# Kernel optimization log

Measured on AMD Instinct MI355X. Metric: run time of the kernel, lower is better.

The kernel has to match this reference:

```python
import jax, jax.numpy as jnp
import numpy as np

N, E, T, CIN, COUT = 20000, 160000, 8, 64, 128


def setup_inputs() -> dict:
    key = jax.random.key(0)
    ks = jax.random.split(key, 8)
    x = jax.random.normal(ks[0], (T, N, CIN), jnp.float32)
    edge_index = jax.random.randint(ks[1], (2, E), 0, N)
    edge_weight = jax.random.normal(ks[2], (E,), jnp.float32)
    # temporal Conv1d: kernel 3, xavier-ish small init (gain=0.1 in source)
    tconv_w = jax.random.normal(ks[3], (COUT, CIN, 3), jnp.float32) * 0.02
    tconv_b = jnp.zeros((COUT,), jnp.float32)
    ln_g = jnp.ones((COUT,), jnp.float32)
    ln_b = jnp.zeros((COUT,), jnp.float32)
    # residual 1x1 Conv1d (in != out channels)
    res_w = jax.random.normal(ks[4], (COUT, CIN), jnp.float32) * 0.05
    res_b = jnp.zeros((COUT,), jnp.float32)
    # GCNConv linear weight [out, in] and bias
    gcn_w = jax.random.normal(ks[5], (COUT, COUT), jnp.float32) * 0.05
    gcn_b = jnp.zeros((COUT,), jnp.float32)
    return dict(x=x, edge_index=edge_index, edge_weight=edge_weight,
                tconv_w=tconv_w, tconv_b=tconv_b, ln_g=ln_g, ln_b=ln_b,
                res_w=res_w, res_b=res_b, gcn_w=gcn_w, gcn_b=gcn_b)


def reference(x, edge_index, edge_weight, tconv_w, tconv_b, ln_g, ln_b,
              res_w, res_b, gcn_w, gcn_b):
    Tn, Nn, _ = x.shape
    xc = jnp.transpose(x, (1, 2, 0))  # [N, Cin, T]
    # temporal conv over T (kernel 3, pad 1)
    h = jax.lax.conv_general_dilated(
        xc, tconv_w, window_strides=(1,), padding=[(1, 1)],
        dimension_numbers=('NCH', 'OIH', 'NCH')) + tconv_b[None, :, None]
    h = jnp.transpose(h, (0, 2, 1))  # [N, T, Cout]
    # LayerNorm over channel dim
    mu = h.mean(-1, keepdims=True)
    var = ((h - mu) ** 2).mean(-1, keepdims=True)
    h = (h - mu) * jax.lax.rsqrt(var + 1e-5) * ln_g + ln_b
    h = jax.nn.relu(h)
    # 1x1 residual conv: [N,Cin,T] x [Cout,Cin] -> [N,T,Cout]
    res = jnp.einsum('nct,oc->nto', xc, res_w) + res_b
    xcmb = h + res  # [N, T, Cout]
    # --- GCNConv (PyG): softmax edge weights, self-loops, sym-normalize ---
    ew = jax.nn.softmax(edge_weight)  # softmax over all edges (dim=0)
    row, col = edge_index[0], edge_index[1]
    sl = jnp.arange(Nn)
    row_f = jnp.concatenate([row, sl])
    col_f = jnp.concatenate([col, sl])
    w_f = jnp.concatenate([ew, jnp.ones((Nn,), ew.dtype)])  # self-loop weight 1
    deg = jax.ops.segment_sum(w_f, col_f, num_segments=Nn)
    dinv = jnp.where(deg > 0, jax.lax.rsqrt(jnp.maximum(deg, 1e-12)), 0.0)
    norm = dinv[row_f] * w_f * dinv[col_f]  # [E+N]
    xt = jnp.einsum('ntc,oc->nto', xcmb, gcn_w)  # linear transform, all T at once
    msg = norm[:, None, None] * xt[row_f]        # gather sources: [E+N, T, Cout]
    agg = jax.ops.segment_sum(msg, col_f, num_segments=Nn) + gcn_b
    out = jax.nn.relu(agg)  # [N, T, Cout]
    return jnp.transpose(out, (1, 0, 2))  # [T, N, Cout] == stacked per-t list
```

## Files before the change

### kernel.cpp

```cpp
#include <hip/hip_runtime.h>
#include <math.h>

#define N_NODES 20000
#define E_EDGES 160000
#define T_STEPS 8
#define C_IN    64
#define C_OUT   128

typedef __bf16 bf16x8 __attribute__((ext_vector_type(8)));
typedef float  f32x4  __attribute__((ext_vector_type(4)));
#define MFMA16(a, b, c) __builtin_amdgcn_mfma_f32_16x16x32_bf16((a), (b), (c), 0, 0, 0)

__device__ __forceinline__ unsigned short f2u(float f) {
  __bf16 b = (__bf16)f;
  return __builtin_bit_cast(unsigned short, b);
}
__device__ __forceinline__ unsigned int pack2(float lo, float hi) {
  return (unsigned int)f2u(lo) | ((unsigned int)f2u(hi) << 16);
}

__device__ __forceinline__ float wredSum(float v) {
#pragma unroll
  for (int d = 32; d > 0; d >>= 1) v += __shfl_xor(v, d, 64);
  return v;
}
__device__ __forceinline__ float wredMax(float v) {
#pragma unroll
  for (int d = 32; d > 0; d >>= 1) v = fmaxf(v, __shfl_xor(v, d, 64));
  return v;
}
__device__ __forceinline__ int wredSumI(int v) {
#pragma unroll
  for (int d = 32; d > 0; d >>= 1) v += __shfl_xor(v, d, 64);
  return v;
}
__device__ __forceinline__ float bredSum(float v, float* sm4) {
  __syncthreads();
  v = wredSum(v);
  const int lane = threadIdx.x & 63, wid = threadIdx.x >> 6;
  if (lane == 0) sm4[wid] = v;
  __syncthreads();
  return sm4[0] + sm4[1] + sm4[2] + sm4[3];
}
__device__ __forceinline__ float bredMax(float v, float* sm4) {
  __syncthreads();
  v = wredMax(v);
  const int lane = threadIdx.x & 63, wid = threadIdx.x >> 6;
  if (lane == 0) sm4[wid] = v;
  __syncthreads();
  return fmaxf(fmaxf(sm4[0], sm4[1]), fmaxf(sm4[2], sm4[3]));
}
__device__ __forceinline__ int bredSumI(int v, int* sm4) {
  __syncthreads();
  v = wredSumI(v);
  const int lane = threadIdx.x & 63, wid = threadIdx.x >> 6;
  if (lane == 0) sm4[wid] = v;
  __syncthreads();
  return sm4[0] + sm4[1] + sm4[2] + sm4[3];
}

__global__ __launch_bounds__(256) void k_esoft(const float* __restrict__ w,
                                               float* __restrict__ pm, float* __restrict__ ps) {
  __shared__ float sm4[4];
  float m = -3.4e38f, s = 0.f;
  for (int i = blockIdx.x * 256 + threadIdx.x; i < E_EDGES; i += 256 * 256) {
    const float xw = w[i];
    if (xw > m) { s = s * expf(m - xw) + 1.f; m = xw; }
    else        { s += expf(xw - m); }
  }
  const float M = bredMax(m, sm4);
  const float sp = (s > 0.f) ? s * expf(m - M) : 0.f;
  const float S = bredSum(sp, sm4);
  if (threadIdx.x == 0) { pm[blockIdx.x] = M; ps[blockIdx.x] = S; }
}

__global__ __launch_bounds__(256) void k_edge(const float* __restrict__ w, const int* __restrict__ ei,
                                              const float* __restrict__ pm, const float* __restrict__ ps,
                                              float* __restrict__ ewv, float* __restrict__ deg,
                                              int* __restrict__ cnt) {
  __shared__ float sm4[4];
  const float mloc = pm[threadIdx.x];
  const float mx   = bredMax(mloc, sm4);
  const float sp   = ps[threadIdx.x] * expf(mloc - mx);
  const float sum  = bredSum(sp, sm4);
  const int e = blockIdx.x * 256 + threadIdx.x;
  const float v = expf(w[e] - mx) / sum;
  ewv[e] = v;
  const int c = ei[E_EDGES + e];
  atomicAdd(&deg[c], v);
  atomicAdd(&cnt[c], 1);
}

__global__ __launch_bounds__(256) void k_scan2(const int* __restrict__ cnt, const float* __restrict__ deg,
                                               float* __restrict__ dinv, int* __restrict__ off,
                                               int* __restrict__ cursor) {
  __shared__ int smI[4];
  __shared__ int wpart[4];
  const int tid = threadIdx.x, lane = tid & 63, wid = tid >> 6;
  const int i = blockIdx.x * 256 + tid;
  if (i < N_NODES) dinv[i] = rsqrtf(deg[i]);
  int part = 0;
  const int lim = blockIdx.x * 256;
  for (int j = tid; j < lim; j += 256) part += cnt[j];
  const int base = bredSumI(part, smI);
  const int v = (i < N_NODES) ? cnt[i] : 0;
  int s = v;
#pragma unroll
  for (int d = 1; d < 64; d <<= 1) { const int u = __shfl_up(s, d, 64); if (lane >= d) s += u; }
  if (lane == 63) wpart[wid] = s;
  __syncthreads();
  int add = base;
#pragma unroll
  for (int wv = 0; wv < 4; ++wv) if (wv < wid) add += wpart[wv];
  if (i < N_NODES) { const int excl = add + (s - v); off[i] = excl; cursor[i] = excl; }
  if (i == N_NODES - 1) off[N_NODES] = E_EDGES;
}

__global__ __launch_bounds__(256) void k_norm_scatter(const int* __restrict__ ei, const float* __restrict__ ewv,
                                                      const float* __restrict__ dinv, const float* __restrict__ qsc,
                                                      int* __restrict__ cursor, uint2* __restrict__ srcnrm) {
  const int e = blockIdx.x * 256 + threadIdx.x;
  const int r = ei[e], c = ei[E_EDGES + e];
  const float mul = dinv[r] * ewv[e] * dinv[c] * qsc[r];
  const int pos = atomicAdd(&cursor[c], 1);
  srcnrm[pos] = make_uint2((unsigned int)r, __builtin_bit_cast(unsigned int, mul));
}

__global__ __launch_bounds__(256) void k_wprep(const float* __restrict__ tconv_w, const float* __restrict__ res_w,
                                               const float* __restrict__ gcn_w, unsigned int* __restrict__ Bf,
                                               float* __restrict__ deg, int* __restrict__ cnt) {
  const int gid = blockIdx.x * 256 + threadIdx.x;
  if (gid < N_NODES) { deg[gid] = 1.0f; cnt[gid] = 0; }
  float v0, v1;
  if (gid < 12288) {
    const int reg = gid & 3, l = (gid >> 2) & 63, ct = (gid >> 8) & 7, ks = gid >> 11;
    const int o = ct * 16 + (l & 15);
    const int k0 = ks * 32 + ((l >> 4) & 3) * 8 + reg * 2;
    const int c0 = k0 & 63, tap0 = k0 >> 6;
    const int c1 = (k0 + 1) & 63, tap1 = (k0 + 1) >> 6;
    v0 = tconv_w[o * 192 + c0 * 3 + tap0];
    v1 = tconv_w[o * 192 + c1 * 3 + tap1];
  } else if (gid < 16384) {
    const int g = gid - 12288;
    const int reg = g & 3, l = (g >> 2) & 63, ct = (g >> 8) & 7, ks = g >> 11;
    const int o = ct * 16 + (l & 15);
    const int k0 = ks * 32 + ((l >> 4) & 3) * 8 + reg * 2;
    v0 = res_w[o * 64 + k0];
    v1 = res_w[o * 64 + k0 + 1];
  } else {
    const int g = gid - 16384;
    const int reg = g & 3, l = (g >> 2) & 63, ct = (g >> 8) & 7, ks = g >> 11;
    const int o = ct * 16 + (l & 15);
    const int k0 = ks * 32 + ((l >> 4) & 3) * 8 + reg * 2;
    v0 = gcn_w[o * 128 + k0];
    v1 = gcn_w[o * 128 + k0 + 1];
  }
  Bf[gid] = pack2(v0, v1);
}

#define XS_NODE 720
#define XS_SLOT 72
#define AS2_STRIDE 136
__global__ __launch_bounds__(256, 2) void k_fuse(const float* __restrict__ x,
                                                 const float* __restrict__ tconv_b,
                                                 const float* __restrict__ ln_g, const float* __restrict__ ln_b,
                                                 const float* __restrict__ res_b,
                                                 const unsigned int* __restrict__ Bf,
                                                 unsigned char* __restrict__ xq,
                                                 float* __restrict__ qsc) {
  const int tid = threadIdx.x, lane = tid & 63, w = tid >> 6;
  const int l15 = lane & 15, lg = lane >> 4;
  const int n0 = blockIdx.x * 16;

  __shared__ __align__(16) unsigned short XsAs[128 * AS2_STRIDE];
  unsigned short* Xs  = XsAs;
  unsigned short* As2 = XsAs;
  __shared__ float psum[4][128], psq[4][128];
  __shared__ float smu[128], srs[128];
  __shared__ unsigned int nmax[16];

  if (tid < 16) nmax[tid] = 0u;

#pragma unroll
  for (int p = 0; p < 8; ++p) {
    const int chunk = p * 256 + tid;
    const int tq = chunk >> 8, nn = (chunk >> 4) & 15, c4 = chunk & 15;
    const float4 v = *(const float4*)(x + ((size_t)tq * N_NODES + n0 + nn) * C_IN + c4 * 4);
    uint2 pk; pk.x = pack2(v.x, v.y); pk.y = pack2(v.z, v.w);
    *(uint2*)&Xs[nn * XS_NODE + (tq + 1) * XS_SLOT + c4 * 4] = pk;
  }
#pragma unroll
  for (int p = 0; p < 3; ++p) {
    const int i = p * 256 + tid;
    if (i < 576) {
      const int nn = i / 36;
      const int r = i - nn * 36;
      const int sl = (r < 18) ? 0 : 9;
      const int of = ((r < 18) ? r : r - 18) * 4;
      *(uint2*)&Xs[nn * XS_NODE + sl * XS_SLOT + of] = make_uint2(0u, 0u);
    }
  }

  const uint4* Bf4 = (const uint4*)Bf;
  uint4 Bc[2][6], Br[2][2];
#pragma unroll
  for (int ct = 0; ct < 2; ++ct) {
    const int ctg = w * 2 + ct;
#pragma unroll
    for (int ks = 0; ks < 6; ++ks) Bc[ct][ks] = Bf4[(ks * 8 + ctg) * 64 + lane];
#pragma unroll
    for (int ks = 0; ks < 2; ++ks) Br[ct][ks] = Bf4[3072 + (ks * 8 + ctg) * 64 + lane];
  }
  float cb[2], rb[2], gv[2], bv[2];
#pragma unroll
  for (int ct = 0; ct < 2; ++ct) {
    const int col = w * 32 + ct * 16 + l15;
    cb[ct] = tconv_b[col]; rb[ct] = res_b[col]; gv[ct] = ln_g[col]; bv[ct] = ln_b[col];
  }
  __syncthreads();

  f32x4 accC[8][2], accR[8][2];
#pragma unroll
  for (int rt = 0; rt < 8; ++rt)
#pragma unroll
    for (int ct = 0; ct < 2; ++ct) { accC[rt][ct] = (f32x4)0.f; accR[rt][ct] = (f32x4)0.f; }

#pragma unroll
  for (int ks = 0; ks < 6; ++ks) {
    bf16x8 af[8];
    const int slot = (l15 & 7) + (ks >> 1);
    const int koff = slot * XS_SLOT + (ks & 1) * 32 + lg * 8;
#pragma unroll
    for (int rt = 0; rt < 8; ++rt) {
      const int node = rt * 2 + (l15 >> 3);
      af[rt] = *(const bf16x8*)&Xs[node * XS_NODE + koff];
    }
#pragma unroll
    for (int rt = 0; rt < 8; ++rt)
#pragma unroll
      for (int ct = 0; ct < 2; ++ct)
        accC[rt][ct] = MFMA16(af[rt], __builtin_bit_cast(bf16x8, Bc[ct][ks]), accC[rt][ct]);
    if (ks == 2 || ks == 3) {
#pragma unroll
      for (int rt = 0; rt < 8; ++rt)
#pragma unroll
        for (int ct = 0; ct < 2; ++ct)
          accR[rt][ct] = MFMA16(af[rt], __builtin_bit_cast(bf16x8, Br[ct][ks - 2]), accR[rt][ct]);
    }
  }

#pragma unroll
  for (int rt = 0; rt < 8; ++rt) {
    float s[4], s2[4];
#pragma unroll
    for (int j = 0; j < 4; ++j) {
      const float h0 = accC[rt][0][j] + cb[0];
      const float h1 = accC[rt][1][j] + cb[1];
      accC[rt][0][j] = h0; accC[rt][1][j] = h1;
      s[j] = h0 + h1; s2[j] = h0 * h0 + h1 * h1;
    }
#pragma unroll
    for (int d = 1; d < 16; d <<= 1)
#pragma unroll
      for (int j = 0; j < 4; ++j) { s[j] += __shfl_xor(s[j], d, 64); s2[j] += __shfl_xor(s2[j], d, 64); }
    if (l15 == 0)
#pragma unroll
      for (int j = 0; j < 4; ++j) {
        psum[w][rt * 16 + lg * 4 + j] = s[j];
        psq[w][rt * 16 + lg * 4 + j] = s2[j];
      }
  }
  __syncthreads();
  if (tid < 128) {
    const float S  = psum[0][tid] + psum[1][tid] + psum[2][tid] + psum[3][tid];
    const float S2 = psq[0][tid] + psq[1][tid] + psq[2][tid] + psq[3][tid];
    const float mu = S * (1.f / 128.f);
    const float var = S2 * (1.f / 128.f) - mu * mu;
    smu[tid] = mu; srs[tid] = rsqrtf(var + 1e-5f);
  }
  __syncthreads();

#pragma unroll
  for (int rt = 0; rt < 8; ++rt)
#pragma unroll
    for (int j = 0; j < 4; ++j) {
      const int row = rt * 16 + lg * 4 + j;
      const float mu = smu[row], rs = srs[row];
      const int sw = ((row >> 3) & 1) << 4;
#pragma unroll
      for (int ct = 0; ct < 2; ++ct) {
        float xc = (accC[rt][ct][j] - mu) * rs * gv[ct] + bv[ct];
        xc = fmaxf(xc, 0.f) + accR[rt][ct][j] + rb[ct];
        const int col = w * 32 + ct * 16 + l15;
        As2[row * AS2_STRIDE + (col ^ sw)] = f2u(xc);
      }
    }
  __syncthreads();

  uint4 Bg[2][4];
#pragma unroll
  for (int ct = 0; ct < 2; ++ct)
#pragma unroll
    for (int ks = 0; ks < 4; ++ks) Bg[ct][ks] = Bf4[4096 + (ks * 8 + (w * 2 + ct)) * 64 + lane];

  f32x4 acc[8][2];
#pragma unroll
  for (int rt = 0; rt < 8; ++rt)
#pragma unroll
    for (int ct = 0; ct < 2; ++ct) acc[rt][ct] = (f32x4)0.f;

  const int swr = ((l15 >> 3) & 1) << 4;
#pragma unroll
  for (int ks = 0; ks < 4; ++ks) {
    bf16x8 af[8];
    const int koff = (ks * 32 + lg * 8) ^ swr;
#pragma unroll
    for (int rt = 0; rt < 8; ++rt)
      af[rt] = *(const bf16x8*)&As2[(rt * 16 + l15) * AS2_STRIDE + koff];
#pragma unroll
    for (int rt = 0; rt < 8; ++rt)
#pragma unroll
      for (int ct = 0; ct < 2; ++ct)
        acc[rt][ct] = MFMA16(af[rt], __builtin_bit_cast(bf16x8, Bg[ct][ks]), acc[rt][ct]);
  }

#pragma unroll
  for (int rt = 0; rt < 8; ++rt) {
    const int nn = rt * 2 + (lg >> 1);
    float m = 0.f;
#pragma unroll
    for (int ct = 0; ct < 2; ++ct)
#pragma unroll
      for (int j = 0; j < 4; ++j) m = fmaxf(m, fabsf(acc[rt][ct][j]));
    atomicMax(&nmax[nn], __builtin_bit_cast(unsigned int, m));
  }
  __syncthreads();
  if (tid < 16) qsc[n0 + tid] = __builtin_bit_cast(float, nmax[tid]) * (1.f / 127.f);

  const int t0 = (lg & 1) * 4;
#pragma unroll
  for (int rt = 0; rt < 8; ++rt) {
    const int nn = rt * 2 + (lg >> 1);
    const size_t n = (size_t)(n0 + nn);
    const float mx = __builtin_bit_cast(float, nmax[nn]);
    const float inv = (mx > 0.f) ? 127.f / mx : 0.f;
#pragma unroll
    for (int ct = 0; ct < 2; ++ct) {
      const int col = w * 32 + ct * 16 + l15;
      unsigned int pk8 = 0;
#pragma unroll
      for (int j = 0; j < 4; ++j) {
        const int q = (int)rintf(acc[rt][ct][j] * inv) + 128;
        pk8 |= ((unsigned int)q) << (8 * j);
      }
      *(unsigned int*)(xq + (n * C_OUT + col) * T_STEPS + t0) = pk8;
    }
  }
}

__global__ __launch_bounds__(256) void k_agg(const unsigned char* __restrict__ xq,
                                             const float* __restrict__ qsc,
                                             const uint2* __restrict__ srcnrm,
                                             const int* __restrict__ off, const float* __restrict__ dinv,
                                             const float* __restrict__ gcn_b, float* __restrict__ out) {
  const int tid = threadIdx.x, lane = tid & 63, w = tid >> 6;
  const int j = blockIdx.x * 4 + w;
  const int s = off[j], e = off[j + 1];
  const float d2 = dinv[j] * dinv[j];

  float acc[2][8];
#pragma unroll
  for (int h = 0; h < 2; ++h)
#pragma unroll
    for (int t = 0; t < 8; ++t) acc[h][t] = 0.f;

  float summul;
  {
    const float mul = d2 * qsc[j];
    summul = mul;
    const uint2 qa = *(const uint2*)(xq + ((size_t)j * C_OUT + lane) * T_STEPS);
    const uint2 qb = *(const uint2*)(xq + ((size_t)j * C_OUT + 64 + lane) * T_STEPS);
#pragma unroll
    for (int tt = 0; tt < 4; ++tt) {
      acc[0][tt]     = fmaf((float)((qa.x >> (8 * tt)) & 0xffu), mul, acc[0][tt]);
      acc[0][4 + tt] = fmaf((float)((qa.y >> (8 * tt)) & 0xffu), mul, acc[0][4 + tt]);
      acc[1][tt]     = fmaf((float)((qb.x >> (8 * tt)) & 0xffu), mul, acc[1][tt]);
      acc[1][4 + tt] = fmaf((float)((qb.y >> (8 * tt)) & 0xffu), mul, acc[1][4 + tt]);
    }
  }

  for (int cs = s; cs < e; cs += 64) {
    const uint2 sn = srcnrm[cs + lane];
    const int   rv = (int)sn.x;
    const float mv = __builtin_bit_cast(float, sn.y);
    const int cnt = min(64, e - cs);
    for (int k = 0; k < cnt; ++k) {
      const int   r   = __shfl(rv, k, 64);
      const float mul = __shfl(mv, k, 64);
      summul += mul;
      const uint2 qa = *(const uint2*)(xq + ((size_t)r * C_OUT + lane) * T_STEPS);
      const uint2 qb = *(const uint2*)(xq + ((size_t)r * C_OUT + 64 + lane) * T_STEPS);
#pragma unroll
      for (int tt = 0; tt < 4; ++tt) {
        acc[0][tt]     = fmaf((float)((qa.x >> (8 * tt)) & 0xffu), mul, acc[0][tt]);
        acc[0][4 + tt] = fmaf((float)((qa.y >> (8 * tt)) & 0xffu), mul, acc[0][4 + tt]);
        acc[1][tt]     = fmaf((float)((qb.x >> (8 * tt)) & 0xffu), mul, acc[1][tt]);
        acc[1][4 + tt] = fmaf((float)((qb.y >> (8 * tt)) & 0xffu), mul, acc[1][4 + tt]);
      }
    }
  }

  const float corr = 128.f * summul;
  const float b0 = gcn_b[lane], b1 = gcn_b[64 + lane];
#pragma unroll
  for (int h = 0; h < 2; ++h) {
    const float bo = h ? b1 : b0;
#pragma unroll
    for (int t = 0; t < 8; ++t) {
      const float v = acc[h][t] - corr + bo;
      out[((size_t)t * N_NODES + j) * C_OUT + h * 64 + lane] = fmaxf(v, 0.f);
    }
  }
}

extern "C" void kernel_launch(void* const* d_in, const int* in_sizes, int n_in,
                              void* d_out, int out_size, void* d_ws, size_t ws_size,
                              hipStream_t stream) {
  (void)in_sizes; (void)n_in; (void)out_size; (void)ws_size;
  const float* x       = (const float*)d_in[0];
  const int*   ei      = (const int*)d_in[1];
  const float* ewt     = (const float*)d_in[2];
  const float* tconv_w = (const float*)d_in[3];
  const float* tconv_b = (const float*)d_in[4];
  const float* ln_g    = (const float*)d_in[5];
  const float* ln_b    = (const float*)d_in[6];
  const float* res_w   = (const float*)d_in[7];
  const float* res_b   = (const float*)d_in[8];
  const float* gcn_w   = (const float*)d_in[9];
  const float* gcn_b   = (const float*)d_in[10];
  float* out = (float*)d_out;

  unsigned char* xq = (unsigned char*)d_ws;
  float* qsc  = (float*)(xq + (size_t)N_NODES * C_OUT * T_STEPS);
  unsigned int* Bf = (unsigned int*)(qsc + N_NODES);
  float* ewv   = (float*)(Bf + 24576);
  float* deg   = ewv + E_EDGES;
  float* dinv  = deg + N_NODES;
  float* pm    = dinv + N_NODES;
  float* ps    = pm + 256;
  int*   cnt    = (int*)(ps + 256);
  int*   off    = cnt + N_NODES;
  int*   cursor = off + N_NODES + 1;
  uint2* srcnrm = (uint2*)(((size_t)(cursor + N_NODES) + 15) & ~(size_t)15);

  const int nblk = (N_NODES + 255) / 256;
  const int eblk = E_EDGES / 256;

  k_wprep<<<96, 256, 0, stream>>>(tconv_w, res_w, gcn_w, Bf, deg, cnt);
  k_esoft<<<256, 256, 0, stream>>>(ewt, pm, ps);
  k_edge<<<eblk, 256, 0, stream>>>(ewt, ei, pm, ps, ewv, deg, cnt);
  k_scan2<<<nblk, 256, 0, stream>>>(cnt, deg, dinv, off, cursor);
  k_fuse<<<1250, 256, 0, stream>>>(x, tconv_b, ln_g, ln_b, res_b, Bf, xq, qsc);
  k_norm_scatter<<<eblk, 256, 0, stream>>>(ei, ewv, dinv, qsc, cursor, srcnrm);
  k_agg<<<N_NODES / 4, 256, 0, stream>>>(xq, qsc, srcnrm, off, dinv, gcn_b, out);
}
```

Measured before the change: 142.5 us.

## Fold residual conv into GCN weight, halve fuse tile, simplify agg loop

Precomputes W_gcn·W_res and W_gcn·res_b in the weight-prep kernel, so the residual branch is added inside the GCN GEMM and the separate residual accumulators and epilogue add go away. k_fuse now handles 8 nodes per block instead of 16 with separate Xs/As2 shared buffers, and launches twice as many blocks. The aggregation loop drops the shuffle-broadcast batching and loads each edge record directly. This cuts register and MFMA pressure in k_fuse and raises occupancy, at the cost of a serial per-thread 128-long dot product in the prep kernel and a change in bf16 rounding order.

```diff
diff --git a/kernel.cpp b/kernel.cpp
--- a/kernel.cpp
+++ b/kernel.cpp
@@ -127,10 +127,16 @@
 }
 
 __global__ __launch_bounds__(256) void k_wprep(const float* __restrict__ tconv_w, const float* __restrict__ res_w,
-                                               const float* __restrict__ gcn_w, unsigned int* __restrict__ Bf,
+                                               const float* __restrict__ gcn_w, const float* __restrict__ res_b,
+                                               unsigned int* __restrict__ Bf, float* __restrict__ c2,
                                                float* __restrict__ deg, int* __restrict__ cnt) {
   const int gid = blockIdx.x * 256 + threadIdx.x;
   if (gid < N_NODES) { deg[gid] = 1.0f; cnt[gid] = 0; }
+  if (gid < 128) {
+    float s = 0.f;
+    for (int o = 0; o < 128; ++o) s += gcn_w[gid * 128 + o] * res_b[o];
+    c2[gid] = s;
+  }
   float v0, v1;
   if (gid < 12288) {
     const int reg = gid & 3, l = (gid >> 2) & 63, ct = (gid >> 8) & 7, ks = gid >> 11;
@@ -143,10 +149,15 @@
   } else if (gid < 16384) {
     const int g = gid - 12288;
     const int reg = g & 3, l = (g >> 2) & 63, ct = (g >> 8) & 7, ks = g >> 11;
-    const int o = ct * 16 + (l & 15);
+    const int q = ct * 16 + (l & 15);
     const int k0 = ks * 32 + ((l >> 4) & 3) * 8 + reg * 2;
-    v0 = res_w[o * 64 + k0];
-    v1 = res_w[o * 64 + k0 + 1];
+    float a0 = 0.f, a1 = 0.f;
+    for (int o = 0; o < 128; ++o) {
+      const float gq = gcn_w[q * 128 + o];
+      a0 = fmaf(gq, res_w[o * 64 + k0], a0);
+      a1 = fmaf(gq, res_w[o * 64 + k0 + 1], a1);
+    }
+    v0 = a0; v1 = a1;
   } else {
     const int g = gid - 16384;
     const int reg = g & 3, l = (g >> 2) & 63, ct = (g >> 8) & 7, ks = g >> 11;
@@ -164,35 +175,34 @@
 __global__ __launch_bounds__(256, 2) void k_fuse(const float* __restrict__ x,
                                                  const float* __restrict__ tconv_b,
                                                  const float* __restrict__ ln_g, const float* __restrict__ ln_b,
-                                                 const float* __restrict__ res_b,
                                                  const unsigned int* __restrict__ Bf,
+                                                 const float* __restrict__ c2,
                                                  unsigned char* __restrict__ xq,
                                                  float* __restrict__ qsc) {
   const int tid = threadIdx.x, lane = tid & 63, w = tid >> 6;
   const int l15 = lane & 15, lg = lane >> 4;
-  const int n0 = blockIdx.x * 16;
-
-  __shared__ __align__(16) unsigned short XsAs[128 * AS2_STRIDE];
-  unsigned short* Xs  = XsAs;
-  unsigned short* As2 = XsAs;
-  __shared__ float psum[4][128], psq[4][128];
-  __shared__ float smu[128], srs[128];
-  __shared__ unsigned int nmax[16];
-
-  if (tid < 16) nmax[tid] = 0u;
-
-#pragma unroll
-  for (int p = 0; p < 8; ++p) {
+  const int n0 = blockIdx.x * 8;
+
+  __shared__ __align__(16) unsigned short Xs[8 * XS_NODE];
+  __shared__ __align__(16) unsigned short As2[64 * AS2_STRIDE];
+  __shared__ float psum[4][64], psq[4][64];
+  __shared__ float smu[64], srs[64];
+  __shared__ unsigned int nmax[8];
+
+  if (tid < 8) nmax[tid] = 0u;
+
+#pragma unroll
+  for (int p = 0; p < 4; ++p) {
     const int chunk = p * 256 + tid;
-    const int tq = chunk >> 8, nn = (chunk >> 4) & 15, c4 = chunk & 15;
+    const int tq = chunk >> 7, nn = (chunk >> 4) & 7, c4 = chunk & 15;
     const float4 v = *(const float4*)(x + ((size_t)tq * N_NODES + n0 + nn) * C_IN + c4 * 4);
     uint2 pk; pk.x = pack2(v.x, v.y); pk.y = pack2(v.z, v.w);
     *(uint2*)&Xs[nn * XS_NODE + (tq + 1) * XS_SLOT + c4 * 4] = pk;
   }
 #pragma unroll
-  for (int p = 0; p < 3; ++p) {
+  for (int p = 0; p < 2; ++p) {
     const int i = p * 256 + tid;
-    if (i < 576) {
+    if (i < 288) {
       const int nn = i / 36;
       const int r = i - nn * 36;
       const int sl = (r < 18) ? 0 : 9;
@@ -202,55 +212,48 @@
   }
 
   const uint4* Bf4 = (const uint4*)Bf;
-  uint4 Bc[2][6], Br[2][2];
+  uint4 Bc[2][6], Bw2[2][2];
 #pragma unroll
   for (int ct = 0; ct < 2; ++ct) {
     const int ctg = w * 2 + ct;
 #pragma unroll
     for (int ks = 0; ks < 6; ++ks) Bc[ct][ks] = Bf4[(ks * 8 + ctg) * 64 + lane];
 #pragma unroll
-    for (int ks = 0; ks < 2; ++ks) Br[ct][ks] = Bf4[3072 + (ks * 8 + ctg) * 64 + lane];
-  }
-  float cb[2], rb[2], gv[2], bv[2];
+    for (int ks = 0; ks < 2; ++ks) Bw2[ct][ks] = Bf4[3072 + (ks * 8 + ctg) * 64 + lane];
+  }
+  float cb[2], gv[2], bv[2], cc[2];
 #pragma unroll
   for (int ct = 0; ct < 2; ++ct) {
     const int col = w * 32 + ct * 16 + l15;
-    cb[ct] = tconv_b[col]; rb[ct] = res_b[col]; gv[ct] = ln_g[col]; bv[ct] = ln_b[col];
-  }
-  __syncthreads();
-
-  f32x4 accC[8][2], accR[8][2];
-#pragma unroll
-  for (int rt = 0; rt < 8; ++rt)
-#pragma unroll
-    for (int ct = 0; ct < 2; ++ct) { accC[rt][ct] = (f32x4)0.f; accR[rt][ct] = (f32x4)0.f; }
+    cb[ct] = tconv_b[col]; gv[ct] = ln_g[col]; bv[ct] = ln_b[col]; cc[ct] = c2[col];
+  }
+  __syncthreads();
+
+  f32x4 accC[4][2];
+#pragma unroll
+  for (int rt = 0; rt < 4; ++rt)
+#pragma unroll
+    for (int ct = 0; ct < 2; ++ct) accC[rt][ct] = (f32x4)0.f;
 
 #pragma unroll
   for (int ks = 0; ks < 6; ++ks) {
-    bf16x8 af[8];
+    bf16x8 af[4];
     const int slot = (l15 & 7) + (ks >> 1);
     const int koff = slot * XS_SLOT + (ks & 1) * 32 + lg * 8;
 #pragma unroll
-    for (int rt = 0; rt < 8; ++rt) {
+    for (int rt = 0; rt < 4; ++rt) {
       const int node = rt * 2 + (l15 >> 3);
       af[rt] = *(const bf16x8*)&Xs[node * XS_NODE + koff];
     }
 #pragma unroll
-    for (int rt = 0; rt < 8; ++rt)
+    for (int rt = 0; rt < 4; ++rt)
 #pragma unroll
       for (int ct = 0; ct < 2; ++ct)
         accC[rt][ct] = MFMA16(af[rt], __builtin_bit_cast(bf16x8, Bc[ct][ks]), accC[rt][ct]);
-    if (ks == 2 || ks == 3) {
-#pragma unroll
-      for (int rt = 0; rt < 8; ++rt)
-#pragma unroll
-        for (int ct = 0; ct < 2; ++ct)
-          accR[rt][ct] = MFMA16(af[rt], __builtin_bit_cast(bf16x8, Br[ct][ks - 2]), accR[rt][ct]);
-    }
-  }
-
-#pragma unroll
-  for (int rt = 0; rt < 8; ++rt) {
+  }
+
+#pragma unroll
+  for (int rt = 0; rt < 4; ++rt) {
     float s[4], s2[4];
 #pragma unroll
     for (int j = 0; j < 4; ++j) {
@@ -271,7 +274,7 @@
       }
   }
   __syncthreads();
-  if (tid < 128) {
+  if (tid < 64) {
     const float S  = psum[0][tid] + psum[1][tid] + psum[2][tid] + psum[3][tid];
     const float S2 = psq[0][tid] + psq[1][tid] + psq[2][tid] + psq[3][tid];
     const float mu = S * (1.f / 128.f);
@@ -281,7 +284,7 @@
   __syncthreads();
 
 #pragma unroll
-  for (int rt = 0; rt < 8; ++rt)
+  for (int rt = 0; rt < 4; ++rt)
 #pragma unroll
     for (int j = 0; j < 4; ++j) {
       const int row = rt * 16 + lg * 4 + j;
@@ -290,7 +293,7 @@
 #pragma unroll
       for (int ct = 0; ct < 2; ++ct) {
         float xc = (accC[rt][ct][j] - mu) * rs * gv[ct] + bv[ct];
-        xc = fmaxf(xc, 0.f) + accR[rt][ct][j] + rb[ct];
+        xc = fmaxf(xc, 0.f);
         const int col = w * 32 + ct * 16 + l15;
         As2[row * AS2_STRIDE + (col ^ sw)] = f2u(xc);
       }
@@ -303,43 +306,63 @@
 #pragma unroll
     for (int ks = 0; ks < 4; ++ks) Bg[ct][ks] = Bf4[4096 + (ks * 8 + (w * 2 + ct)) * 64 + lane];
 
-  f32x4 acc[8][2];
-#pragma unroll
-  for (int rt = 0; rt < 8; ++rt)
-#pragma unroll
-    for (int ct = 0; ct < 2; ++ct) acc[rt][ct] = (f32x4)0.f;
+  f32x4 accG[4][2];
+#pragma unroll
+  for (int rt = 0; rt < 4; ++rt)
+#pragma unroll
+    for (int ct = 0; ct < 2; ++ct) accG[rt][ct] = (f32x4)0.f;
+
+#pragma unroll
+  for (int ks = 0; ks < 2; ++ks) {
+    bf16x8 af[4];
+    const int koff = ((l15 & 7) + 1) * XS_SLOT + ks * 32 + lg * 8;
+#pragma unroll
+    for (int rt = 0; rt < 4; ++rt) {
+      const int node = rt * 2 + (l15 >> 3);
+      af[rt] = *(const bf16x8*)&Xs[node * XS_NODE + koff];
+    }
+#pragma unroll
+    for (int rt = 0; rt < 4; ++rt)
+#pragma unroll
+      for (int ct = 0; ct < 2; ++ct)
+        accG[rt][ct] = MFMA16(af[rt], __builtin_bit_cast(bf16x8, Bw2[ct][ks]), accG[rt][ct]);
+  }
 
   const int swr = ((l15 >> 3) & 1) << 4;
 #pragma unroll
   for (int ks = 0; ks < 4; ++ks) {
-    bf16x8 af[8];
+    bf16x8 af[4];
     const int koff = (ks * 32 + lg * 8) ^ swr;
 #pragma unroll
-    for (int rt = 0; rt < 8; ++rt)
+    for (int rt = 0; rt < 4; ++rt)
       af[rt] = *(const bf16x8*)&As2[(rt * 16 + l15) * AS2_STRIDE + koff];
 #pragma unroll
-    for (int rt = 0; rt < 8; ++rt)
+    for (int rt = 0; rt < 4; ++rt)
 #pragma unroll
       for (int ct = 0; ct < 2; ++ct)
-        acc[rt][ct] = MFMA16(af[rt], __builtin_bit_cast(bf16x8, Bg[ct][ks]), acc[rt][ct]);
-  }
-
-#pragma unroll
-  for (int rt = 0; rt < 8; ++rt) {
+        accG[rt][ct] = MFMA16(af[rt], __builtin_bit_cast(bf16x8, Bg[ct][ks]), accG[rt][ct]);
+  }
+
+#pragma unroll
+  for (int rt = 0; rt < 4; ++rt) {
+#pragma unroll
+    for (int ct = 0; ct < 2; ++ct)
+#pragma unroll
+      for (int j = 0; j < 4; ++j) accG[rt][ct][j] += cc[ct];
     const int nn = rt * 2 + (lg >> 1);
     float m = 0.f;
 #pragma unroll
     for (int ct = 0; ct < 2; ++ct)
 #pragma unroll
-      for (int j = 0; j < 4; ++j) m = fmaxf(m, fabsf(acc[rt][ct][j]));
+      for (int j = 0; j < 4; ++j) m = fmaxf(m, fabsf(accG[rt][ct][j]));
     atomicMax(&nmax[nn], __builtin_bit_cast(unsigned int, m));
   }
   __syncthreads();
-  if (tid < 16) qsc[n0 + tid] = __builtin_bit_cast(float, nmax[tid]) * (1.f / 127.f);
+  if (tid < 8) qsc[n0 + tid] = __builtin_bit_cast(float, nmax[tid]) * (1.f / 127.f);
 
   const int t0 = (lg & 1) * 4;
 #pragma unroll
-  for (int rt = 0; rt < 8; ++rt) {
+  for (int rt = 0; rt < 4; ++rt) {
     const int nn = rt * 2 + (lg >> 1);
     const size_t n = (size_t)(n0 + nn);
     const float mx = __builtin_bit_cast(float, nmax[nn]);
@@ -350,7 +373,7 @@
       unsigned int pk8 = 0;
 #pragma unroll
       for (int j = 0; j < 4; ++j) {
-        const int q = (int)rintf(acc[rt][ct][j] * inv) + 128;
+        const int q = (int)rintf(accG[rt][ct][j] * inv) + 128;
         pk8 |= ((unsigned int)q) << (8 * j);
       }
       *(unsigned int*)(xq + (n * C_OUT + col) * T_STEPS + t0) = pk8;
@@ -389,24 +412,19 @@
     }
   }
 
-  for (int cs = s; cs < e; cs += 64) {
-    const uint2 sn = srcnrm[cs + lane];
-    const int   rv = (int)sn.x;
-    const float mv = __builtin_bit_cast(float, sn.y);
-    const int cnt = min(64, e - cs);
-    for (int k = 0; k < cnt; ++k) {
-      const int   r   = __shfl(rv, k, 64);
-      const float mul = __shfl(mv, k, 64);
-      summul += mul;
-      const uint2 qa = *(const uint2*)(xq + ((size_t)r * C_OUT + lane) * T_STEPS);
-      const uint2 qb = *(const uint2*)(xq + ((size_t)r * C_OUT + 64 + lane) * T_STEPS);
-#pragma unroll
-      for (int tt = 0; tt < 4; ++tt) {
-        acc[0][tt]     = fmaf((float)((qa.x >> (8 * tt)) & 0xffu), mul, acc[0][tt]);
-        acc[0][4 + tt] = fmaf((float)((qa.y >> (8 * tt)) & 0xffu), mul, acc[0][4 + tt]);
-        acc[1][tt]     = fmaf((float)((qb.x >> (8 * tt)) & 0xffu), mul, acc[1][tt]);
-        acc[1][4 + tt] = fmaf((float)((qb.y >> (8 * tt)) & 0xffu), mul, acc[1][4 + tt]);
-      }
+  for (int k = s; k < e; ++k) {
+    const uint2 sn = srcnrm[k];
+    const int r = (int)sn.x;
+    const float mul = __builtin_bit_cast(float, sn.y);
+    summul += mul;
+    const uint2 qa = *(const uint2*)(xq + ((size_t)r * C_OUT + lane) * T_STEPS);
+    const uint2 qb = *(const uint2*)(xq + ((size_t)r * C_OUT + 64 + lane) * T_STEPS);
+#pragma unroll
+    for (int tt = 0; tt < 4; ++tt) {
+      acc[0][tt]     = fmaf((float)((qa.x >> (8 * tt)) & 0xffu), mul, acc[0][tt]);
+      acc[0][4 + tt] = fmaf((float)((qa.y >> (8 * tt)) & 0xffu), mul, acc[0][4 + tt]);
+      acc[1][tt]     = fmaf((float)((qb.x >> (8 * tt)) & 0xffu), mul, acc[1][tt]);
+      acc[1][4 + tt] = fmaf((float)((qb.y >> (8 * tt)) & 0xffu), mul, acc[1][4 + tt]);
     }
   }
 
@@ -442,7 +460,8 @@
 
   unsigned char* xq = (unsigned char*)d_ws;
   float* qsc  = (float*)(xq + (size_t)N_NODES * C_OUT * T_STEPS);
-  unsigned int* Bf = (unsigned int*)(qsc + N_NODES);
+  float* c2   = qsc + N_NODES;
+  unsigned int* Bf = (unsigned int*)(c2 + 128);
   float* ewv   = (float*)(Bf + 24576);
   float* deg   = ewv + E_EDGES;
   float* dinv  = deg + N_NODES;
@@ -456,11 +475,11 @@
   const int nblk = (N_NODES + 255) / 256;
   const int eblk = E_EDGES / 256;
 
-  k_wprep<<<96, 256, 0, stream>>>(tconv_w, res_w, gcn_w, Bf, deg, cnt);
+  k_wprep<<<96, 256, 0, stream>>>(tconv_w, res_w, gcn_w, res_b, Bf, c2, deg, cnt);
   k_esoft<<<256, 256, 0, stream>>>(ewt, pm, ps);
   k_edge<<<eblk, 256, 0, stream>>>(ewt, ei, pm, ps, ewv, deg, cnt);
   k_scan2<<<nblk, 256, 0, stream>>>(cnt, deg, dinv, off, cursor);
-  k_fuse<<<1250, 256, 0, stream>>>(x, tconv_b, ln_g, ln_b, res_b, Bf, xq, qsc);
+  k_fuse<<<2500, 256, 0, stream>>>(x, tconv_b, ln_g, ln_b, Bf, c2, xq, qsc);
   k_norm_scatter<<<eblk, 256, 0, stream>>>(ei, ewv, dinv, qsc, cursor, srcnrm);
   k_agg<<<N_NODES / 4, 256, 0, stream>>>(xq, qsc, srcnrm, off, dinv, gcn_b, out);
 }
```

Result: no change. 142.5 us (-0.0%).
